# Kernel optimization log

Measured on AMD Instinct MI355X. Metric: run time of the kernel, lower is better.

Reference implementation:

```python
import jax, jax.numpy as jnp
import numpy as np

B, S, D = 4, 2048, 1024
H = 16
HS = D // H  # 64


def setup_inputs() -> dict:
    key = jax.random.key(0)
    ks = jax.random.split(key, 6)
    scale = 1.0 / np.sqrt(D)
    x = jax.random.normal(ks[0], (B, S, D), dtype=jnp.float32)
    # per-head projection weights, stacked: [H, D, HS]
    Wq = jax.random.normal(ks[1], (H, D, HS), dtype=jnp.float32) * scale
    Wk = jax.random.normal(ks[2], (H, D, HS), dtype=jnp.float32) * scale
    Wv = jax.random.normal(ks[3], (H, D, HS), dtype=jnp.float32) * scale
    Wo = jax.random.normal(ks[4], (D, D), dtype=jnp.float32) * scale
    bo = jax.random.normal(ks[5], (D,), dtype=jnp.float32) * 0.01
    return {"x": x, "Wq": Wq, "Wk": Wk, "Wv": Wv, "Wo": Wo, "bo": bo}


def reference(x, Wq, Wk, Wv, Wo, bo):
    # Per-head dense projections (no bias): [B,S,D] x [H,D,HS] -> [B,H,S,HS]
    q = jnp.einsum('bsd,hde->bhse', x, Wq)
    k = jnp.einsum('bsd,hde->bhse', x, Wk)
    v = jnp.einsum('bsd,hde->bhse', x, Wv)
    # scaled dot-product scores: [B,H,S,S]
    scores = jnp.einsum('bhse,bhte->bhst', q, k) / jnp.sqrt(jnp.asarray(HS, dtype=x.dtype))
    # causal mask (lower triangular kept)
    causal = jnp.tril(jnp.ones((S, S), dtype=bool))
    scores = jnp.where(causal, scores, -jnp.inf)
    attn = jax.nn.softmax(scores, axis=-1)
    # dropout is identity at inference (rate handled as 0)
    out = jnp.einsum('bhst,bhte->bhse', attn, v)  # [B,H,S,HS]
    # concat heads: [B,S,H*HS] = [B,S,D]
    out = jnp.transpose(out, (0, 2, 1, 3)).reshape(B, S, D)
    return out @ Wo + bo
```

## Files before the change

### kernel.cpp

```cpp
#include <hip/hip_runtime.h>
#include <hip/hip_bf16.h>
#include <stdint.h>

#define NB 4
#define NS 2048
#define ND 1024
#define NH 16
#define NHS 64
#define NEG_BIG (-1e30f)
#define Q_SCALE 0.18033688011112042f

typedef __bf16 bf16x8 __attribute__((ext_vector_type(8)));
typedef float floatx4 __attribute__((ext_vector_type(4)));
typedef short s16x4 __attribute__((ext_vector_type(4)));

#if defined(__has_builtin)
#if __has_builtin(__builtin_amdgcn_mfma_f32_16x16x16bf16_1k)
#define HAVE_MFMA1K 1
#endif
#endif
#ifndef HAVE_MFMA1K
#define HAVE_MFMA1K 0
#endif

static constexpr size_t WSLAB = (size_t)NH * ND * NHS;
static constexpr size_t QSLAB = (size_t)NB * NH * NS * NHS;
static constexpr size_t XSLAB = (size_t)NB * NS * ND;

__device__ __forceinline__ uint16_t f2b(float f) {
    union { __hip_bfloat16 h; uint16_t u; } cv;
    cv.h = __float2bfloat16(f);
    return cv.u;
}

__device__ __forceinline__ void gll16(const void* g, void* l) {
  __builtin_amdgcn_global_load_lds(
      (__attribute__((address_space(1))) void*)(uintptr_t)g,
      (__attribute__((address_space(3))) void*)(uintptr_t)l,
      16, 0, 0);
}

__global__ __launch_bounds__(256) void k_prep(
    const float* __restrict__ x, const float* __restrict__ Wq,
    const float* __restrict__ Wk, const float* __restrict__ Wv,
    const float* __restrict__ Wo, uint16_t* __restrict__ xb,
    uint16_t* __restrict__ wt) {
  __shared__ __align__(16) uint16_t T[64][72];
  int bid = blockIdx.x;
  int tid = threadIdx.x;
  if (bid < 4096) {
    size_t i0 = ((size_t)bid * 256 + tid) * 8;
    float4 f0 = *(const float4*)&x[i0];
    float4 f1 = *(const float4*)&x[i0 + 4];
    __align__(16) uint16_t tmp[8];
    tmp[0] = f2b(f0.x); tmp[1] = f2b(f0.y); tmp[2] = f2b(f0.z); tmp[3] = f2b(f0.w);
    tmp[4] = f2b(f1.x); tmp[5] = f2b(f1.y); tmp[6] = f2b(f1.z); tmp[7] = f2b(f1.w);
    *(uint4*)&xb[i0] = *(uint4*)tmp;
    return;
  }
  bid -= 4096;
  const float* src; uint16_t* dst;
  int srcStride, dstStride, r0, c0;
  if (bid < 768) {
    int mat = bid >> 8;
    int rem = bid & 255;
    int h = rem >> 4, dt = rem & 15;
    const float* W = (mat == 0) ? Wq : (mat == 1) ? Wk : Wv;
    src = W + (size_t)h * (ND * NHS);
    dst = wt + (size_t)mat * WSLAB + (size_t)h * (NHS * ND);
    srcStride = NHS; dstStride = ND;
    r0 = dt * 64; c0 = 0;
  } else {
    int rem = bid - 768;
    int dt = rem >> 4, et = rem & 15;
    src = Wo; dst = wt + 3 * WSLAB;
    srcStride = ND; dstStride = ND;
    r0 = dt * 64; c0 = et * 64;
  }
  for (int u = tid; u < 1024; u += 256) {
    int row = u >> 4, cq = u & 15;
    float4 f = *(const float4*)&src[(size_t)(r0 + row) * srcStride + c0 + cq * 4];
    uint16_t* p = &T[row][cq * 4];
    p[0] = f2b(f.x); p[1] = f2b(f.y); p[2] = f2b(f.z); p[3] = f2b(f.w);
  }
  __syncthreads();
  for (int u = tid; u < 512; u += 256) {
    int c = u >> 3, cg = u & 7;
    __align__(16) uint16_t tmp[8];
    for (int j = 0; j < 8; j++) tmp[j] = T[cg * 8 + j][c];
    *(uint4*)&dst[(size_t)(c0 + c) * dstStride + r0 + cg * 8] = *(uint4*)tmp;
  }
}

__global__ __launch_bounds__(512, 2) void k_qkv(
    const uint16_t* __restrict__ xb, const uint16_t* __restrict__ wt,
    uint16_t* __restrict__ qk, uint16_t* __restrict__ vt) {
  __shared__ __align__(16) uint16_t L[49152];

  int bid = blockIdx.x;
  int xcd = bid & 7, idx = bid >> 3;
  int mtile = xcd * 8 + (idx & 7);
  int ntile = idx >> 3;
  int m0 = mtile * 128;
  int n0 = ntile * 256;

  int tid = threadIdx.x;
  int wave = tid >> 6, lane = tid & 63, quad = lane >> 4, l16 = lane & 15;
  int wr = wave >> 2, wc = wave & 3;

  const uint16_t* pA = xb + (size_t)(m0 + (tid >> 2)) * ND + (tid & 3) * 8;
  const uint16_t* pB = wt + (size_t)(n0 + (tid >> 2)) * ND + (tid & 3) * 8;
  const int stOff = wave * 512;

  const int offA = (wr * 64 + l16) * 32 + quad * 8;
  const int offB = (wc * 64 + l16) * 32 + quad * 8;

  floatx4 acc[4][4];
  #pragma unroll
  for (int i = 0; i < 4; i++)
    #pragma unroll
    for (int j = 0; j < 4; j++) acc[i][j] = (floatx4){0.f, 0.f, 0.f, 0.f};

#define STAGE_A(A_)                                                             \
  do {                                                                          \
    int a_ = (A_);                                                              \
    if (a_ < 32) {                                                              \
      gll16(pA + (a_ >> 1) * 64 + (a_ & 1) * 32, &L[(a_ & 3) * 4096 + stOff]);  \
    }                                                                           \
  } while (0)
#define STAGE_B(A_)                                                             \
  do {                                                                          \
    int a_ = (A_);                                                              \
    if (a_ < 32) {                                                              \
      const uint16_t* g_ = pB + (a_ >> 1) * 64 + (a_ & 1) * 32;                 \
      uint16_t* l_ = &L[16384 + (a_ & 3) * 8192 + stOff];                       \
      gll16(g_, l_);                                                            \
      gll16(g_ + 128 * ND, l_ + 4096);                                          \
    }                                                                           \
  } while (0)

#define PH_BAR()                         \
  do {                                   \
    asm volatile("" ::: "memory");       \
    __builtin_amdgcn_s_barrier();        \
    asm volatile("" ::: "memory");       \
  } while (0)

  STAGE_A(0); STAGE_B(0);
  STAGE_A(1); STAGE_B(1);
  STAGE_A(2); STAGE_B(2);
  asm volatile("s_waitcnt vmcnt(6)" ::: "memory");
  PH_BAR();

#define MFMA16()                                                                          \
  _Pragma("unroll")                                                                       \
  for (int mt_ = 0; mt_ < 4; mt_++)                                                       \
    _Pragma("unroll")                                                                     \
    for (int nt_ = 0; nt_ < 4; nt_++)                                                     \
      acc[mt_][nt_] = __builtin_amdgcn_mfma_f32_16x16x32_bf16(af[mt_], bfr[nt_], acc[mt_][nt_], 0, 0, 0)

  for (int t = 0; t < 16; ++t) {
    int sA0 = (t & 1) * 8192;
    int sB0 = 16384 + (t & 1) * 16384;
    {
      bf16x8 af[4], bfr[4];
      #pragma unroll
      for (int i = 0; i < 4; i++) {
        af[i]  = *(const bf16x8*)&L[sA0 + offA + i * 512];
        bfr[i] = *(const bf16x8*)&L[sB0 + offB + i * 512];
      }
      STAGE_A(2 * t + 3); STAGE_B(2 * t + 3);
      PH_BAR();
      __builtin_amdgcn_s_setprio(1);
      MFMA16();
      __builtin_amdgcn_s_setprio(0);
      if (t < 15) { asm volatile("s_waitcnt vmcnt(6)" ::: "memory"); }
      else        { asm volatile("s_waitcnt vmcnt(0)" ::: "memory"); }
      PH_BAR();
    }
    {
      bf16x8 af[4], bfr[4];
      #pragma unroll
      for (int i = 0; i < 4; i++) {
        af[i]  = *(const bf16x8*)&L[sA0 + 4096 + offA + i * 512];
        bfr[i] = *(const bf16x8*)&L[sB0 + 8192 + offB + i * 512];
      }
      STAGE_A(2 * t + 4); STAGE_B(2 * t + 4);
      PH_BAR();
      __builtin_amdgcn_s_setprio(1);
      MFMA16();
      __builtin_amdgcn_s_setprio(0);
      if (t < 14)       { asm volatile("s_waitcnt vmcnt(6)" ::: "memory"); }
      else if (t == 14) { asm volatile("s_waitcnt vmcnt(3)" ::: "memory"); }
      PH_BAR();
    }
  }
#undef MFMA16
#undef STAGE_A
#undef STAGE_B
#undef PH_BAR

  int matid = n0 >> 10;
  if (matid == 2) {
    int hh = ((n0 - 2048) >> 6) + wc;
    int b = m0 >> 11;
    #pragma unroll
    for (int nt = 0; nt < 4; nt++) {
      int e = nt * 16 + l16;
      uint16_t* vrow = vt + ((size_t)(b * 16 + hh) * 64 + e) * NS;
      #pragma unroll
      for (int mt = 0; mt < 4; mt++) {
        __align__(8) uint16_t t4v[4];
        #pragma unroll
        for (int r = 0; r < 4; r++) t4v[r] = f2b(acc[mt][nt][r]);
        int s = (m0 & 2047) + wr * 64 + mt * 16 + quad * 4;
        *(uint2*)&vrow[s] = *(uint2*)t4v;
      }
    }
  } else {
    float scale = (matid == 0) ? Q_SCALE : 1.0f;
    uint16_t* base = qk + (size_t)matid * QSLAB;
    int hh = ((n0 & 1023) >> 6) + wc;
    int b = m0 >> 11;
    #pragma unroll
    for (int mt = 0; mt < 4; mt++) {
      int s = (m0 & 2047) + wr * 64 + mt * 16 + quad * 4;
      size_t rbase = ((size_t)(b * 16 + hh) * NS + s) * NHS;
      #pragma unroll
      for (int nt = 0; nt < 4; nt++)
        #pragma unroll
        for (int r = 0; r < 4; r++)
          base[rbase + (size_t)r * NHS + nt * 16 + l16] = f2b(acc[mt][nt][r] * scale);
    }
  }
}

#if HAVE_MFMA1K
__global__ __launch_bounds__(256, 4) void k_attn(
    const uint16_t* __restrict__ Q, const uint16_t* __restrict__ K,
    const uint16_t* __restrict__ VT, uint16_t* __restrict__ Y) {
  __shared__ __align__(16) uint16_t Ks[64][72];
  __shared__ __align__(16) uint16_t Vs[64][72];
  int bh = blockIdx.y;
  int b = bh >> 4, h = bh & 15;
  int ta = blockIdx.x;
  int tb = 31 - ta;
  const uint16_t* Qp = Q + (size_t)bh * (NS * NHS);
  const uint16_t* Kp = K + (size_t)bh * (NS * NHS);
  const uint16_t* Vp = VT + (size_t)bh * (NS * NHS);
  int tid = threadIdx.x;
  int wv = tid >> 6, lane = tid & 63, quad = lane >> 4, l16 = lane & 15;

  int row0 = tid >> 3, cg0 = tid & 7;
  int row1 = (tid + 256) >> 3, cg1 = tid & 7;

  int rA = ta * 64 + wv * 16 + l16;
  int rB = tb * 64 + wv * 16 + l16;
  bf16x8 aqA0 = *(const bf16x8*)&Qp[(size_t)rA * NHS + quad * 8];
  bf16x8 aqA1 = *(const bf16x8*)&Qp[(size_t)rA * NHS + 32 + quad * 8];
  bf16x8 aqB0 = *(const bf16x8*)&Qp[(size_t)rB * NHS + quad * 8];
  bf16x8 aqB1 = *(const bf16x8*)&Qp[(size_t)rB * NHS + 32 + quad * 8];

  float lAs = 0.f, lBs = 0.f;
  floatx4 oA[4], oB[4];
  for (int et = 0; et < 4; et++) {
    oA[et] = (floatx4){0.f, 0.f, 0.f, 0.f};
    oB[et] = (floatx4){0.f, 0.f, 0.f, 0.f};
  }

  uint4 rk0, rk1, rv0, rv1;
  rk0 = *(const uint4*)&Kp[(size_t)(0 * 64 + row0) * NHS + cg0 * 8];
  rk1 = *(const uint4*)&Kp[(size_t)(0 * 64 + row1) * NHS + cg1 * 8];
  rv0 = *(const uint4*)&Vp[(size_t)row0 * NS + 0 * 64 + cg0 * 8];
  rv1 = *(const uint4*)&Vp[(size_t)row1 * NS + 0 * 64 + cg1 * 8];

  for (int kt = 0; kt <= tb; kt++) {
    bool doA = (kt <= ta);
    __syncthreads();
    *(uint4*)&Ks[row0][cg0 * 8] = rk0;
    *(uint4*)&Ks[row1][cg1 * 8] = rk1;
    *(uint4*)&Vs[row0][cg0 * 8] = rv0;
    *(uint4*)&Vs[row1][cg1 * 8] = rv1;
    __syncthreads();
    if (kt < tb) {
      rk0 = *(const uint4*)&Kp[(size_t)((kt + 1) * 64 + row0) * NHS + cg0 * 8];
      rk1 = *(const uint4*)&Kp[(size_t)((kt + 1) * 64 + row1) * NHS + cg1 * 8];
      rv0 = *(const uint4*)&Vp[(size_t)row0 * NS + (kt + 1) * 64 + cg0 * 8];
      rv1 = *(const uint4*)&Vp[(size_t)row1 * NS + (kt + 1) * 64 + cg1 * 8];
    }

    s16x4 pbA[4], pbB[4];
    for (int ct = 0; ct < 4; ct++) {
      bf16x8 kb0 = *(const bf16x8*)&Ks[ct * 16 + l16][quad * 8];
      bf16x8 kb1 = *(const bf16x8*)&Ks[ct * 16 + l16][32 + quad * 8];
      int key = kt * 64 + ct * 16 + quad * 4;
      floatx4 c = (floatx4){0.f, 0.f, 0.f, 0.f};
      c = __builtin_amdgcn_mfma_f32_16x16x32_bf16(kb0, aqB0, c, 0, 0, 0);
      c = __builtin_amdgcn_mfma_f32_16x16x32_bf16(kb1, aqB1, c, 0, 0, 0);
      for (int r = 0; r < 4; r++) {
        float s = (kt == tb && key + r > rB) ? NEG_BIG : c[r];
        float p = __builtin_amdgcn_exp2f(s);
        lBs += p;
        pbB[ct][r] = (short)f2b(p);
      }
      if (doA) {
        floatx4 d = (floatx4){0.f, 0.f, 0.f, 0.f};
        d = __builtin_amdgcn_mfma_f32_16x16x32_bf16(kb0, aqA0, d, 0, 0, 0);
        d = __builtin_amdgcn_mfma_f32_16x16x32_bf16(kb1, aqA1, d, 0, 0, 0);
        for (int r = 0; r < 4; r++) {
          float s = (kt == ta && key + r > rA) ? NEG_BIG : d[r];
          float p = __builtin_amdgcn_exp2f(s);
          lAs += p;
          pbA[ct][r] = (short)f2b(p);
        }
      }
    }
    for (int et = 0; et < 4; et++)
      for (int ct = 0; ct < 4; ct++) {
        s16x4 va = *(const s16x4*)&Vs[et * 16 + l16][ct * 16 + quad * 4];
        oB[et] = __builtin_amdgcn_mfma_f32_16x16x16bf16_1k(va, pbB[ct], oB[et], 0, 0, 0);
        if (doA)
          oA[et] = __builtin_amdgcn_mfma_f32_16x16x16bf16_1k(va, pbA[ct], oA[et], 0, 0, 0);
      }
  }
  lAs += __shfl_xor(lAs, 16, 64); lAs += __shfl_xor(lAs, 32, 64);
  lBs += __shfl_xor(lBs, 16, 64); lBs += __shfl_xor(lBs, 32, 64);
  float invA = 1.f / lAs, invB = 1.f / lBs;
  uint16_t* yb = Y + (size_t)b * NS * ND + (size_t)h * NHS;
  for (int et = 0; et < 4; et++) {
    __align__(8) uint16_t tA[4], tB[4];
    for (int r = 0; r < 4; r++) {
      tA[r] = f2b(oA[et][r] * invA);
      tB[r] = f2b(oB[et][r] * invB);
    }
    *(uint2*)&yb[(size_t)rA * ND + et * 16 + quad * 4] = *(uint2*)tA;
    *(uint2*)&yb[(size_t)rB * ND + et * 16 + quad * 4] = *(uint2*)tB;
  }
}
#else
__global__ __launch_bounds__(256) void k_attn(
    const uint16_t* __restrict__ Q, const uint16_t* __restrict__ K,
    const uint16_t* __restrict__ VT, uint16_t* __restrict__ Y) {
  __shared__ __align__(16) uint16_t Ks[64][72];
  __shared__ __align__(16) uint16_t Vs[64][72];
  __shared__ __align__(16) uint16_t Ps[4][2][16][72];
  int bh = blockIdx.y;
  int b = bh >> 4, h = bh & 15;
  int ta = blockIdx.x;
  int tb = 31 - ta;
  const uint16_t* Qp = Q + (size_t)bh * (NS * NHS);
  const uint16_t* Kp = K + (size_t)bh * (NS * NHS);
  const uint16_t* Vp = VT + (size_t)bh * (NS * NHS);
  int tid = threadIdx.x;
  int wv = tid >> 6, lane = tid & 63, quad = lane >> 4, l16 = lane & 15;

  int rA = ta * 64 + wv * 16 + l16;
  int rB = tb * 64 + wv * 16 + l16;
  bf16x8 aqA0 = *(const bf16x8*)&Qp[(size_t)rA * NHS + quad * 8];
  bf16x8 aqA1 = *(const bf16x8*)&Qp[(size_t)rA * NHS + 32 + quad * 8];
  bf16x8 aqB0 = *(const bf16x8*)&Qp[(size_t)rB * NHS + quad * 8];
  bf16x8 aqB1 = *(const bf16x8*)&Qp[(size_t)rB * NHS + 32 + quad * 8];

  float lA[4] = {0.f, 0.f, 0.f, 0.f}, lB[4] = {0.f, 0.f, 0.f, 0.f};
  floatx4 oA[4], oB[4];
  for (int ct = 0; ct < 4; ct++) {
    oA[ct] = (floatx4){0.f, 0.f, 0.f, 0.f};
    oB[ct] = (floatx4){0.f, 0.f, 0.f, 0.f};
  }
  for (int kt = 0; kt <= tb; kt++) {
    bool doA = (kt <= ta);
    __syncthreads();
    for (int u = tid; u < 512; u += 256) {
      int row = u >> 3, cg = u & 7;
      *(uint4*)&Ks[row][cg * 8] =
          *(const uint4*)&Kp[(size_t)(kt * 64 + row) * NHS + cg * 8];
    }
    for (int u = tid; u < 512; u += 256) {
      int row = u >> 3, cg = u & 7;
      *(uint4*)&Vs[row][cg * 8] =
          *(const uint4*)&Vp[(size_t)row * NS + kt * 64 + cg * 8];
    }
    __syncthreads();
    floatx4 sA[4], sB[4];
    for (int ct = 0; ct < 4; ct++) {
      bf16x8 kb0 = *(const bf16x8*)&Ks[ct * 16 + l16][quad * 8];
      bf16x8 kb1 = *(const bf16x8*)&Ks[ct * 16 + l16][32 + quad * 8];
      floatx4 c = (floatx4){0.f, 0.f, 0.f, 0.f};
      c = __builtin_amdgcn_mfma_f32_16x16x32_bf16(aqB0, kb0, c, 0, 0, 0);
      c = __builtin_amdgcn_mfma_f32_16x16x32_bf16(aqB1, kb1, c, 0, 0, 0);
      sB[ct] = c;
      if (doA) {
        floatx4 d = (floatx4){0.f, 0.f, 0.f, 0.f};
        d = __builtin_amdgcn_mfma_f32_16x16x32_bf16(aqA0, kb0, d, 0, 0, 0);
        d = __builtin_amdgcn_mfma_f32_16x16x32_bf16(aqA1, kb1, d, 0, 0, 0);
        sA[ct] = d;
      }
    }
    if (kt == tb) {
      int qrb = tb * 64 + wv * 16 + quad * 4;
      for (int ct = 0; ct < 4; ct++) {
        int kg = kt * 64 + ct * 16 + l16;
        for (int r = 0; r < 4; r++)
          sB[ct][r] = (kg <= qrb + r) ? sB[ct][r] : NEG_BIG;
      }
    }
    if (doA && kt == ta) {
      int qrb = ta * 64 + wv * 16 + quad * 4;
      for (int ct = 0; ct < 4; ct++) {
        int kg = kt * 64 + ct * 16 + l16;
        for (int r = 0; r < 4; r++)
          sA[ct][r] = (kg <= qrb + r) ? sA[ct][r] : NEG_BIG;
      }
    }
    for (int ct = 0; ct < 4; ct++)
      for (int r = 0; r < 4; r++) {
        float p = __builtin_amdgcn_exp2f(sB[ct][r]);
        lB[r] += p;
        Ps[wv][1][quad * 4 + r][ct * 16 + l16] = f2b(p);
      }
    if (doA)
      for (int ct = 0; ct < 4; ct++)
        for (int r = 0; r < 4; r++) {
          float p = __builtin_amdgcn_exp2f(sA[ct][r]);
          lA[r] += p;
          Ps[wv][0][quad * 4 + r][ct * 16 + l16] = f2b(p);
        }
    bf16x8 apB0 = *(const bf16x8*)&Ps[wv][1][l16][quad * 8];
    bf16x8 apB1 = *(const bf16x8*)&Ps[wv][1][l16][32 + quad * 8];
    bf16x8 apA0, apA1;
    if (doA) {
      apA0 = *(const bf16x8*)&Ps[wv][0][l16][quad * 8];
      apA1 = *(const bf16x8*)&Ps[wv][0][l16][32 + quad * 8];
    }
    for (int ct = 0; ct < 4; ct++) {
      bf16x8 vb0 = *(const bf16x8*)&Vs[ct * 16 + l16][quad * 8];
      bf16x8 vb1 = *(const bf16x8*)&Vs[ct * 16 + l16][32 + quad * 8];
      oB[ct] = __builtin_amdgcn_mfma_f32_16x16x32_bf16(apB0, vb0, oB[ct], 0, 0, 0);
      oB[ct] = __builtin_amdgcn_mfma_f32_16x16x32_bf16(apB1, vb1, oB[ct], 0, 0, 0);
      if (doA) {
        oA[ct] = __builtin_amdgcn_mfma_f32_16x16x32_bf16(apA0, vb0, oA[ct], 0, 0, 0);
        oA[ct] = __builtin_amdgcn_mfma_f32_16x16x32_bf16(apA1, vb1, oA[ct], 0, 0, 0);
      }
    }
  }
  for (int off = 1; off < 16; off <<= 1)
    for (int r = 0; r < 4; r++) {
      lA[r] += __shfl_xor(lA[r], off, 64);
      lB[r] += __shfl_xor(lB[r], off, 64);
    }
  uint16_t* yb = Y + (size_t)b * NS * ND + (size_t)h * NHS;
  for (int ct = 0; ct < 4; ct++)
    for (int r = 0; r < 4; r++) {
      int sA_ = ta * 64 + wv * 16 + quad * 4 + r;
      int sB_ = tb * 64 + wv * 16 + quad * 4 + r;
      yb[(size_t)sA_ * ND + ct * 16 + l16] = f2b(oA[ct][r] / lA[r]);
      yb[(size_t)sB_ * ND + ct * 16 + l16] = f2b(oB[ct][r] / lB[r]);
    }
}
#endif

__global__ __launch_bounds__(256) void k_proj(
    const uint16_t* __restrict__ y, const uint16_t* __restrict__ wot,
    const float* __restrict__ bo, float* __restrict__ out) {
  __shared__ __align__(16) uint16_t As[128 * 64];
  __shared__ __align__(16) uint16_t Bs[128 * 64];
  int m0 = blockIdx.x * 128;
  int n0 = blockIdx.y * 128;
  int tid = threadIdx.x;
  int wv = tid >> 6, lane = tid & 63, quad = lane >> 4, l16 = lane & 15;
  int wr = wv >> 1, wc = wv & 1;
  int srow = lane >> 3, scol = lane & 7;

  floatx4 acc[4][4];
  for (int i = 0; i < 4; i++)
    for (int j = 0; j < 4; j++) acc[i][j] = (floatx4){0.f, 0.f, 0.f, 0.f};

  for (int k0 = 0; k0 < ND; k0 += 64) {
    __syncthreads();
    for (int j = 0; j < 4; j++) {
      int rg = wv * 4 + j;
      int r = rg * 8 + srow;
      gll16(&y[(size_t)(m0 + r) * ND + k0 + scol * 8], &As[rg * 512]);
      gll16(&wot[(size_t)(n0 + r) * ND + k0 + scol * 8], &Bs[rg * 512]);
    }
    __syncthreads();
    for (int kk = 0; kk < 2; kk++) {
      bf16x8 af[4], bfr[4];
      for (int t = 0; t < 4; t++) {
        af[t]  = *(const bf16x8*)&As[(wr * 64 + t * 16 + l16) * 64 + kk * 32 + quad * 8];
        bfr[t] = *(const bf16x8*)&Bs[(wc * 64 + t * 16 + l16) * 64 + kk * 32 + quad * 8];
      }
      for (int mt = 0; mt < 4; mt++)
        for (int nt = 0; nt < 4; nt++)
          acc[mt][nt] = __builtin_amdgcn_mfma_f32_16x16x32_bf16(af[mt], bfr[nt], acc[mt][nt], 0, 0, 0);
    }
  }
  for (int mt = 0; mt < 4; mt++)
    for (int nt = 0; nt < 4; nt++)
      for (int r = 0; r < 4; r++) {
        int s = m0 + wr * 64 + mt * 16 + quad * 4 + r;
        int n = n0 + wc * 64 + nt * 16 + l16;
        out[(size_t)s * ND + n] = acc[mt][nt][r] + bo[n];
      }
}

extern "C" void kernel_launch(void* const* d_in, const int* in_sizes, int n_in,
                              void* d_out, int out_size, void* d_ws, size_t ws_size,
                              hipStream_t stream) {
  const float* x  = (const float*)d_in[0];
  const float* Wq = (const float*)d_in[1];
  const float* Wk = (const float*)d_in[2];
  const float* Wv = (const float*)d_in[3];
  const float* Wo = (const float*)d_in[4];
  const float* bo = (const float*)d_in[5];
  uint16_t* ws = (uint16_t*)d_ws;

  uint16_t* wt = ws;
  uint16_t* xb = ws + 4 * WSLAB;
  uint16_t* q  = xb + XSLAB;
  uint16_t* k  = q + QSLAB;
  uint16_t* vt = k + QSLAB;
  uint16_t* y  = vt + QSLAB;

  k_prep<<<dim3(5120), dim3(256), 0, stream>>>(x, Wq, Wk, Wv, Wo, xb, wt);
  k_qkv<<<dim3(768), dim3(512), 0, stream>>>(xb, wt, q, vt);
  k_attn<<<dim3(16, NB * NH), dim3(256), 0, stream>>>(q, k, vt, y);
  k_proj<<<dim3(64, 8), dim3(256), 0, stream>>>(y, wt + 3 * WSLAB, bo, (float*)d_out);
}
```

Measured before the change: 256.7 us.

## Shrink QKV GEMM tile to 128x128 with XOR-swizzled LDS and 4-stage ring

```diff
diff --git a/kernel.cpp b/kernel.cpp
--- a/kernel.cpp
+++ b/kernel.cpp
@@ -92,50 +92,44 @@
   }
 }
 
-__global__ __launch_bounds__(512, 2) void k_qkv(
+__global__ __launch_bounds__(512, 4) void k_qkv(
     const uint16_t* __restrict__ xb, const uint16_t* __restrict__ wt,
     uint16_t* __restrict__ qk, uint16_t* __restrict__ vt) {
-  __shared__ __align__(16) uint16_t L[49152];
+  __shared__ __align__(16) uint16_t L[32768];
 
   int bid = blockIdx.x;
   int xcd = bid & 7, idx = bid >> 3;
   int mtile = xcd * 8 + (idx & 7);
   int ntile = idx >> 3;
   int m0 = mtile * 128;
-  int n0 = ntile * 256;
+  int n0 = ntile * 128;
 
   int tid = threadIdx.x;
   int wave = tid >> 6, lane = tid & 63, quad = lane >> 4, l16 = lane & 15;
   int wr = wave >> 2, wc = wave & 3;
 
-  const uint16_t* pA = xb + (size_t)(m0 + (tid >> 2)) * ND + (tid & 3) * 8;
-  const uint16_t* pB = wt + (size_t)(n0 + (tid >> 2)) * ND + (tid & 3) * 8;
+  int swc = ((tid & 3) ^ ((tid >> 4) & 3)) * 8;
+  const uint16_t* pA = xb + (size_t)(m0 + (tid >> 2)) * ND + swc;
+  const uint16_t* pB = wt + (size_t)(n0 + (tid >> 2)) * ND + swc;
   const int stOff = wave * 512;
 
-  const int offA = (wr * 64 + l16) * 32 + quad * 8;
-  const int offB = (wc * 64 + l16) * 32 + quad * 8;
-
-  floatx4 acc[4][4];
+  const int rq = (quad ^ (l16 >> 2)) * 8;
+  const int offA = (wr * 64 + l16) * 32 + rq;
+  const int offB = (wc * 32 + l16) * 32 + rq;
+
+  floatx4 acc[4][2];
   #pragma unroll
   for (int i = 0; i < 4; i++)
     #pragma unroll
-    for (int j = 0; j < 4; j++) acc[i][j] = (floatx4){0.f, 0.f, 0.f, 0.f};
-
-#define STAGE_A(A_)                                                             \
+    for (int j = 0; j < 2; j++) acc[i][j] = (floatx4){0.f, 0.f, 0.f, 0.f};
+
+#define STAGE(A_)                                                               \
   do {                                                                          \
     int a_ = (A_);                                                              \
     if (a_ < 32) {                                                              \
-      gll16(pA + (a_ >> 1) * 64 + (a_ & 1) * 32, &L[(a_ & 3) * 4096 + stOff]);  \
-    }                                                                           \
-  } while (0)
-#define STAGE_B(A_)                                                             \
-  do {                                                                          \
-    int a_ = (A_);                                                              \
-    if (a_ < 32) {                                                              \
-      const uint16_t* g_ = pB + (a_ >> 1) * 64 + (a_ & 1) * 32;                 \
-      uint16_t* l_ = &L[16384 + (a_ & 3) * 8192 + stOff];                       \
-      gll16(g_, l_);                                                            \
-      gll16(g_ + 128 * ND, l_ + 4096);                                          \
+      int ko_ = (a_ >> 1) * 64 + (a_ & 1) * 32;                                 \
+      gll16(pA + ko_, &L[(a_ & 3) * 4096 + stOff]);                             \
+      gll16(pB + ko_, &L[16384 + (a_ & 3) * 4096 + stOff]);                     \
     }                                                                           \
   } while (0)
 
@@ -146,67 +140,64 @@
     asm volatile("" ::: "memory");       \
   } while (0)
 
-  STAGE_A(0); STAGE_B(0);
-  STAGE_A(1); STAGE_B(1);
-  STAGE_A(2); STAGE_B(2);
-  asm volatile("s_waitcnt vmcnt(6)" ::: "memory");
+  STAGE(0); STAGE(1); STAGE(2);
+  asm volatile("s_waitcnt vmcnt(4)" ::: "memory");
   PH_BAR();
 
-#define MFMA16()                                                                          \
+#define MFMA8()                                                                           \
   _Pragma("unroll")                                                                       \
   for (int mt_ = 0; mt_ < 4; mt_++)                                                       \
     _Pragma("unroll")                                                                     \
-    for (int nt_ = 0; nt_ < 4; nt_++)                                                     \
+    for (int nt_ = 0; nt_ < 2; nt_++)                                                     \
       acc[mt_][nt_] = __builtin_amdgcn_mfma_f32_16x16x32_bf16(af[mt_], bfr[nt_], acc[mt_][nt_], 0, 0, 0)
 
   for (int t = 0; t < 16; ++t) {
-    int sA0 = (t & 1) * 8192;
-    int sB0 = 16384 + (t & 1) * 16384;
     {
-      bf16x8 af[4], bfr[4];
+      int sA = ((2 * t) & 3) * 4096;
+      int sB = 16384 + ((2 * t) & 3) * 4096;
+      bf16x8 af[4], bfr[2];
       #pragma unroll
-      for (int i = 0; i < 4; i++) {
-        af[i]  = *(const bf16x8*)&L[sA0 + offA + i * 512];
-        bfr[i] = *(const bf16x8*)&L[sB0 + offB + i * 512];
-      }
-      STAGE_A(2 * t + 3); STAGE_B(2 * t + 3);
+      for (int i = 0; i < 4; i++) af[i] = *(const bf16x8*)&L[sA + offA + i * 512];
+      #pragma unroll
+      for (int i = 0; i < 2; i++) bfr[i] = *(const bf16x8*)&L[sB + offB + i * 512];
+      STAGE(2 * t + 3);
       PH_BAR();
       __builtin_amdgcn_s_setprio(1);
-      MFMA16();
+      MFMA8();
       __builtin_amdgcn_s_setprio(0);
-      if (t < 15) { asm volatile("s_waitcnt vmcnt(6)" ::: "memory"); }
+      if (t < 15) { asm volatile("s_waitcnt vmcnt(4)" ::: "memory"); }
       else        { asm volatile("s_waitcnt vmcnt(0)" ::: "memory"); }
       PH_BAR();
     }
     {
-      bf16x8 af[4], bfr[4];
+      int sA = ((2 * t + 1) & 3) * 4096;
+      int sB = 16384 + ((2 * t + 1) & 3) * 4096;
+      bf16x8 af[4], bfr[2];
       #pragma unroll
-      for (int i = 0; i < 4; i++) {
-        af[i]  = *(const bf16x8*)&L[sA0 + 4096 + offA + i * 512];
-        bfr[i] = *(const bf16x8*)&L[sB0 + 8192 + offB + i * 512];
-      }
-      STAGE_A(2 * t + 4); STAGE_B(2 * t + 4);
+      for (int i = 0; i < 4; i++) af[i] = *(const bf16x8*)&L[sA + offA + i * 512];
+      #pragma unroll
+      for (int i = 0; i < 2; i++) bfr[i] = *(const bf16x8*)&L[sB + offB + i * 512];
+      STAGE(2 * t + 4);
       PH_BAR();
       __builtin_amdgcn_s_setprio(1);
-      MFMA16();
+      MFMA8();
       __builtin_amdgcn_s_setprio(0);
-      if (t < 14)       { asm volatile("s_waitcnt vmcnt(6)" ::: "memory"); }
-      else if (t == 14) { asm volatile("s_waitcnt vmcnt(3)" ::: "memory"); }
-      PH_BAR();
-    }
-  }
-#undef MFMA16
-#undef STAGE_A
-#undef STAGE_B
+      if (t < 14)       { asm volatile("s_waitcnt vmcnt(4)" ::: "memory"); }
+      else if (t == 14) { asm volatile("s_waitcnt vmcnt(2)" ::: "memory"); }
+      if (t < 15) PH_BAR();
+    }
+  }
+#undef MFMA8
+#undef STAGE
 #undef PH_BAR
 
   int matid = n0 >> 10;
+  int b = m0 >> 11;
   if (matid == 2) {
-    int hh = ((n0 - 2048) >> 6) + wc;
-    int b = m0 >> 11;
+    int hh = ((n0 - 2048) >> 6) + (wc >> 1);
     #pragma unroll
-    for (int nt = 0; nt < 4; nt++) {
-      int e = nt * 16 + l16;
+    for (int nt = 0; nt < 2; nt++) {
+      int e = (wc & 1) * 32 + nt * 16 + l16;
       uint16_t* vrow = vt + ((size_t)(b * 16 + hh) * 64 + e) * NS;
       #pragma unroll
       for (int mt = 0; mt < 4; mt++) {
@@ -220,17 +211,17 @@
   } else {
     float scale = (matid == 0) ? Q_SCALE : 1.0f;
     uint16_t* base = qk + (size_t)matid * QSLAB;
-    int hh = ((n0 & 1023) >> 6) + wc;
-    int b = m0 >> 11;
+    int hh = ((n0 & 1023) >> 6) + (wc >> 1);
     #pragma unroll
     for (int mt = 0; mt < 4; mt++) {
       int s = (m0 & 2047) + wr * 64 + mt * 16 + quad * 4;
       size_t rbase = ((size_t)(b * 16 + hh) * NS + s) * NHS;
       #pragma unroll
-      for (int nt = 0; nt < 4; nt++)
+      for (int nt = 0; nt < 2; nt++)
         #pragma unroll
         for (int r = 0; r < 4; r++)
-          base[rbase + (size_t)r * NHS + nt * 16 + l16] = f2b(acc[mt][nt][r] * scale);
+          base[rbase + (size_t)r * NHS + (wc & 1) * 32 + nt * 16 + l16] =
+              f2b(acc[mt][nt][r] * scale);
     }
   }
 }
@@ -523,7 +514,7 @@
   uint16_t* y  = vt + QSLAB;
 
   k_prep<<<dim3(5120), dim3(256), 0, stream>>>(x, Wq, Wk, Wv, Wo, xb, wt);
-  k_qkv<<<dim3(768), dim3(512), 0, stream>>>(xb, wt, q, vt);
+  k_qkv<<<dim3(1536), dim3(512), 0, stream>>>(xb, wt, q, vt);
   k_attn<<<dim3(16, NB * NH), dim3(256), 0, stream>>>(q, k, vt, y);
   k_proj<<<dim3(64, 8), dim3(256), 0, stream>>>(y, wt + 3 * WSLAB, bo, (float*)d_out);
 }
```

Measured after the change: 253.2 us. No clear change (-1.3%).
